# Kernel optimization log

Measured on AMD Instinct MI355X. Metric: run time of the kernel, lower is better.

Reference implementation:

```python
import jax, jax.numpy as jnp
import numpy as np

V, N, K, D, H = 100000, 20000, 32, 256, 256


def setup_inputs() -> dict:
    key = jax.random.key(0)
    k1, k2, k3, k4, k5, k6 = jax.random.split(key, 6)
    return {
        "embed_table": jax.random.normal(k1, (V, D), dtype=jnp.float32),
        "node_ids": jax.random.randint(k2, (N,), 0, V, dtype=jnp.int64) if jax.config.jax_enable_x64 else jax.random.randint(k2, (N,), 0, V, dtype=jnp.int32),
        "nb_ids": jax.random.randint(k3, (N, K), 0, V, dtype=jnp.int32),
        "self_weight": jax.random.normal(k4, (D, H), dtype=jnp.float32) / np.sqrt(D),
        "nb_weight": jax.random.normal(k5, (D, H), dtype=jnp.float32) / np.sqrt(D),
        "bias": jax.random.normal(k6, (2 * H,), dtype=jnp.float32),
    }


def reference(embed_table, node_ids, nb_ids, self_weight, nb_weight, bias):
    # gather self embeddings: [N, D]
    self_attr = embed_table[node_ids]
    # gather sampled neighbor embeddings [N, K, D] and mean-pool over K
    nb_attr = jnp.mean(embed_table[nb_ids], axis=1)
    from_self = self_attr @ self_weight          # [N, H]
    from_nb = nb_attr @ nb_weight                # [N, H]
    out = jnp.concatenate((from_self, from_nb), axis=1) + bias  # concat combine
    return jax.nn.relu(out)
```

## Files before the change

kernel.cpp:

```cpp
#include <hip/hip_runtime.h>

#define VV 100000
#define NN 20000
#define KK 32
#define DD 256
#define HH 256
#define BN 16

typedef __attribute__((ext_vector_type(8))) short bf16x8;
typedef __attribute__((ext_vector_type(4))) float f32x4;

__device__ __forceinline__ ushort f2bf(float f) {
    uint u = __float_as_uint(f);
    return (ushort)((u + 0x7FFFu + ((u >> 16) & 1u)) >> 16);
}
__device__ __forceinline__ float bf2f(ushort u) {
    return __uint_as_float(((uint)u) << 16);
}

__global__ __launch_bounds__(256) void k_conv(
    const float* __restrict__ E, ushort* __restrict__ Eb)
{
    const size_t i = ((size_t)blockIdx.x * 256 + threadIdx.x) * 8;
    const f32x4 a = __builtin_nontemporal_load((const f32x4*)&E[i]);
    const f32x4 b = __builtin_nontemporal_load((const f32x4*)&E[i + 4]);
    bf16x8 v;
    v[0] = (short)f2bf(a.x); v[1] = (short)f2bf(a.y);
    v[2] = (short)f2bf(a.z); v[3] = (short)f2bf(a.w);
    v[4] = (short)f2bf(b.x); v[5] = (short)f2bf(b.y);
    v[6] = (short)f2bf(b.z); v[7] = (short)f2bf(b.w);
    *(bf16x8*)&Eb[i] = v;
}

__global__ __launch_bounds__(256) void k_prep_wf(
    const float* __restrict__ Ws, const float* __restrict__ Wn,
    ushort* __restrict__ WTf)
{
    __shared__ float t[256][17];
    const int tid = threadIdx.x;
    const int h   = blockIdx.y;
    const int tt  = blockIdx.x;
    const float* src = h ? Wn : Ws;
    const int h0 = tt * 16;
    const int c = tid & 15, dr = tid >> 4;
    #pragma unroll
    for (int s = 0; s < 16; ++s) {
        const int d = s * 16 + dr;
        t[d][c] = src[(size_t)d * HH + h0 + c];
    }
    __syncthreads();
    const int fl = tid & 63, w = tid >> 6;
    const int r16 = fl & 15, kg = fl >> 4;
    #pragma unroll
    for (int p = 0; p < 2; ++p) {
        const int ks = w + p * 4;
        bf16x8 v;
        #pragma unroll
        for (int e = 0; e < 8; ++e)
            v[e] = (short)f2bf(t[ks * 32 + kg * 8 + e][r16]);
        *(bf16x8*)&WTf[(((size_t)(h * 16 + tt) * 8 + ks) * 64 + fl) * 8] = v;
    }
}

__global__ __launch_bounds__(256) void k_prep_w(
    const float* __restrict__ Ws, const float* __restrict__ Wn,
    ushort* __restrict__ WT)
{
    __shared__ float t[64][65];
    const int tid = threadIdx.x;
    const float* src = (blockIdx.z == 0) ? Ws : Wn;
    ushort* dst = WT + (size_t)blockIdx.z * HH * DD;
    const int d0 = blockIdx.x * 64, h0 = blockIdx.y * 64;

    const int hl = tid & 63, dq = tid >> 6;
    #pragma unroll
    for (int i = 0; i < 16; ++i) {
        const int dl = dq * 16 + i;
        t[dl][hl] = src[(size_t)(d0 + dl) * HH + h0 + hl];
    }
    __syncthreads();
    const int dl = tid & 63, hq = tid >> 6;
    #pragma unroll
    for (int i = 0; i < 16; ++i) {
        const int h2 = hq * 16 + i;
        dst[(size_t)(h0 + h2) * DD + d0 + dl] = f2bf(t[dl][h2]);
    }
}

__global__ __launch_bounds__(256, 4) void k_gatherf(
    const ushort* __restrict__ Eb,
    const int*    __restrict__ node_ids,
    const int*    __restrict__ nb_ids,
    ushort*       __restrict__ A)
{
    const int wv   = __builtin_amdgcn_readfirstlane((int)(threadIdx.x >> 6));
    const int lane = threadIdx.x & 63;
    const int sub  = lane >> 5;
    const int l31  = lane & 31;
    const int g    = blockIdx.x * 4 + wv;
    const int base = g * KK;

    const int srow = node_ids[g];
    bf16x8 r[17];
    r[0] = *(const bf16x8*)&Eb[((size_t)(uint)srow << 8) + l31 * 8];
    #pragma unroll
    for (int j = 1; j <= 16; ++j) {
        const int rlo = nb_ids[base + j - 1];
        const int rhi = nb_ids[base + j + 15];
        const int row = sub ? rhi : rlo;
        r[j] = *(const bf16x8*)&Eb[((size_t)(uint)row << 8) + l31 * 8];
    }

    float acc[8];
    #pragma unroll
    for (int e = 0; e < 8; ++e) acc[e] = 0.f;
    #pragma unroll
    for (int j = 1; j <= 16; ++j) {
        #pragma unroll
        for (int e = 0; e < 8; ++e)
            acc[e] += bf2f((ushort)r[j][e]);
    }
    #pragma unroll
    for (int e = 0; e < 8; ++e)
        acc[e] += __shfl_xor(acc[e], 32);

    const float inv = 1.0f / (float)KK;
    bf16x8 nv;
    #pragma unroll
    for (int e = 0; e < 8; ++e)
        nv[e] = (short)f2bf(acc[e] * inv);

    const int tile = g >> 4, rr = g & 15;
    const int ks = l31 >> 2, kgw = l31 & 3;
    const size_t dst = (((size_t)(tile * 2 + sub) * 8 + ks) * 64 + kgw * 16 + rr) * 8;
    *(bf16x8*)&A[dst] = sub ? nv : r[0];
}

__global__ __launch_bounds__(256, 4) void k_gemmf(
    const ushort* __restrict__ A,
    const ushort* __restrict__ WTf,
    const float*  __restrict__ bias,
    float*        __restrict__ out)
{
    const int wv   = __builtin_amdgcn_readfirstlane((int)(threadIdx.x >> 6));
    const int lane = threadIdx.x & 63;
    const int tile = blockIdx.x;
    const int half = wv >> 1, qt = wv & 1;
    const int r16 = lane & 15, kg = lane >> 4;

    bf16x8 a[8];
    #pragma unroll
    for (int ks = 0; ks < 8; ++ks)
        a[ks] = *(const bf16x8*)&A[(((size_t)(tile * 2 + half) * 8 + ks) * 64 + lane) * 8];

    f32x4 accs[8];
    #pragma unroll
    for (int ct = 0; ct < 8; ++ct) {
        const int t = qt * 8 + ct;
        f32x4 acc = {0.f, 0.f, 0.f, 0.f};
        #pragma unroll
        for (int ks = 0; ks < 8; ++ks) {
            const bf16x8 b = *(const bf16x8*)&WTf[(((size_t)(half * 16 + t) * 8 + ks) * 64 + lane) * 8];
            acc = __builtin_amdgcn_mfma_f32_16x16x32_bf16(a[ks], b, acc, 0, 0, 0);
        }
        accs[ct] = acc;
    }

    #pragma unroll
    for (int ct = 0; ct < 8; ++ct) {
        const int cglob = half * HH + (qt * 8 + ct) * 16 + r16;
        const float bv = bias[cglob];
        #pragma unroll
        for (int r = 0; r < 4; ++r) {
            const float v = accs[ct][r] + bv;
            out[(size_t)(tile * 16 + kg * 4 + r) * (2 * HH) + cglob] = v > 0.f ? v : 0.f;
        }
    }
}

template<int EBF16>
__global__ __launch_bounds__(256, 4) void k_fused(
    const float*  __restrict__ Ef,
    const ushort* __restrict__ Eb,
    const int*    __restrict__ node_ids,
    const int*    __restrict__ nb_ids,
    const ushort* __restrict__ WT,
    const float*  __restrict__ bias,
    float*        __restrict__ out)
{
    __shared__ ushort As[BN][DD];
    __shared__ ushort An[BN][DD];
    const int tid  = threadIdx.x;
    const int wave = tid >> 6;
    const int lane = tid & 63;
    const int g0   = blockIdx.x * BN;

    if (EBF16) {
        const int sub = lane >> 5;
        const int l31 = lane & 31;
        const uint boff = (uint)l31 * 16;
        for (int n = wave; n < BN; n += 4) {
            const int g = g0 + n;
            const int base = g * KK;
            const uint swz = ((uint)(n & 7)) << 4;
            const int srow = node_ids[g];
            const bf16x8 sv = *(const bf16x8*)&Eb[((size_t)(uint)srow << 8) + l31 * 8];
            bf16x8 r[16];
            #pragma unroll
            for (int j = 0; j < 16; ++j) {
                const int rlo = nb_ids[base + 2 * j];
                const int rhi = nb_ids[base + 2 * j + 1];
                const int row = sub ? rhi : rlo;
                r[j] = *(const bf16x8*)&Eb[((size_t)(uint)row << 8) + l31 * 8];
            }
            float acc[8];
            #pragma unroll
            for (int e = 0; e < 8; ++e) acc[e] = 0.f;
            #pragma unroll
            for (int j = 0; j < 16; ++j) {
                #pragma unroll
                for (int e = 0; e < 8; ++e)
                    acc[e] += bf2f((ushort)r[j][e]);
            }
            #pragma unroll
            for (int e = 0; e < 8; ++e)
                acc[e] += __shfl_xor(acc[e], 32);
            const float inv = 1.0f / (float)KK;
            bf16x8 nv;
            #pragma unroll
            for (int e = 0; e < 8; ++e)
                nv[e] = (short)f2bf(acc[e] * inv);
            if (sub == 0) {
                *(bf16x8*)((char*)&As[n][0] + (boff ^ swz)) = sv;
            } else {
                *(bf16x8*)((char*)&An[n][0] + (boff ^ swz)) = nv;
            }
        }
    } else {
        for (int n = wave; n < BN; n += 4) {
            const int g = g0 + n;
            const int srow = node_ids[g];
            const uint swz  = ((uint)(n & 7)) << 4;
            const uint boff = (uint)lane * 8;
            const float4 s = *(const float4*)&Ef[(size_t)srow * DD + lane * 4];
            ushort4 sv = make_ushort4(f2bf(s.x), f2bf(s.y), f2bf(s.z), f2bf(s.w));
            float4 acc = make_float4(0.f, 0.f, 0.f, 0.f);
            #pragma unroll
            for (int k0 = 0; k0 < KK; k0 += 8) {
                float4 r[8];
                #pragma unroll
                for (int j = 0; j < 8; ++j) {
                    const int row = nb_ids[g * KK + k0 + j];
                    r[j] = *(const float4*)&Ef[(size_t)row * DD + lane * 4];
                }
                #pragma unroll
                for (int j = 0; j < 8; ++j) {
                    acc.x += r[j].x; acc.y += r[j].y;
                    acc.z += r[j].z; acc.w += r[j].w;
                }
            }
            const float inv = 1.0f / (float)KK;
            const ushort4 nv = make_ushort4(f2bf(acc.x * inv), f2bf(acc.y * inv),
                                            f2bf(acc.z * inv), f2bf(acc.w * inv));
            *(ushort4*)((char*)&As[n][0] + (boff ^ swz)) = sv;
            *(ushort4*)((char*)&An[n][0] + (boff ^ swz)) = nv;
        }
    }
    __syncthreads();

    const int half = wave >> 1;
    const int colq = (wave & 1) * 128;
    const int r16  = lane & 15;
    const int kg   = lane >> 4;
    const uint rswz = ((uint)(r16 & 7)) << 4;
    const char* Arow = (const char*)(half ? &An[r16][0] : &As[r16][0]);

    bf16x8 a[8];
    #pragma unroll
    for (int ks = 0; ks < 8; ++ks) {
        const uint off = (uint)(ks * 64 + kg * 16);
        a[ks] = *(const bf16x8*)(Arow + (off ^ rswz));
    }

    const ushort* Wb = WT + (size_t)half * HH * DD;
    f32x4 accs[8];
    #pragma unroll
    for (int ct = 0; ct < 8; ++ct) {
        const int c = colq + ct * 16 + r16;
        const ushort* Bb = Wb + (size_t)c * DD + kg * 8;
        f32x4 acc = {0.f, 0.f, 0.f, 0.f};
        #pragma unroll
        for (int ks = 0; ks < 8; ++ks) {
            const bf16x8 b = *(const bf16x8*)(Bb + ks * 32);
            acc = __builtin_amdgcn_mfma_f32_16x16x32_bf16(a[ks], b, acc, 0, 0, 0);
        }
        accs[ct] = acc;
    }

    #pragma unroll
    for (int ct = 0; ct < 8; ++ct) {
        const int cglob = half * HH + colq + ct * 16 + r16;
        const float bv = bias[cglob];
        #pragma unroll
        for (int r = 0; r < 4; ++r) {
            const float v = accs[ct][r] + bv;
            out[(size_t)(g0 + kg * 4 + r) * (2 * HH) + cglob] = v > 0.f ? v : 0.f;
        }
    }
}

__global__ __launch_bounds__(256, 4) void hetegraph_fused_kernel(
    const float* __restrict__ embed, const int* __restrict__ node_ids,
    const int* __restrict__ nb_ids, const float* __restrict__ Ws,
    const float* __restrict__ Wn, const float* __restrict__ bias,
    float* __restrict__ out)
{
    __shared__ float As[BN][DD];
    __shared__ float An[BN][DD];
    const int tid = threadIdx.x, wave = tid >> 6, lane = tid & 63;
    const int g0 = blockIdx.x * BN;
    for (int n = wave; n < BN; n += 4) {
        const int g = g0 + n;
        const int self_row = node_ids[g];
        const float4 s = *(const float4*)&embed[(size_t)self_row * DD + lane * 4];
        float4 acc = make_float4(0.f, 0.f, 0.f, 0.f);
        for (int k0 = 0; k0 < KK; k0 += 8) {
            float4 r[8];
            #pragma unroll
            for (int j = 0; j < 8; ++j) {
                const int row = nb_ids[g * KK + k0 + j];
                r[j] = *(const float4*)&embed[(size_t)row * DD + lane * 4];
            }
            #pragma unroll
            for (int j = 0; j < 8; ++j) {
                acc.x += r[j].x; acc.y += r[j].y; acc.z += r[j].z; acc.w += r[j].w;
            }
        }
        const float inv = 1.0f / (float)KK;
        *(float4*)&As[n][lane * 4] = s;
        float4 m = make_float4(acc.x * inv, acc.y * inv, acc.z * inv, acc.w * inv);
        *(float4*)&An[n][lane * 4] = m;
    }
    __syncthreads();
    const int h = tid;
    {
        float acc[BN];
        #pragma unroll
        for (int n = 0; n < BN; ++n) acc[n] = 0.f;
        for (int d0 = 0; d0 < DD; d0 += 4) {
            const float w0 = Ws[(d0+0)*HH+h], w1 = Ws[(d0+1)*HH+h];
            const float w2 = Ws[(d0+2)*HH+h], w3 = Ws[(d0+3)*HH+h];
            #pragma unroll
            for (int n = 0; n < BN; ++n) {
                const float4 a = *(const float4*)&As[n][d0];
                acc[n] = fmaf(a.x,w0,acc[n]); acc[n] = fmaf(a.y,w1,acc[n]);
                acc[n] = fmaf(a.z,w2,acc[n]); acc[n] = fmaf(a.w,w3,acc[n]);
            }
        }
        const float b = bias[h];
        #pragma unroll
        for (int n = 0; n < BN; ++n) {
            const float v = acc[n] + b;
            out[(size_t)(g0+n)*(2*HH) + h] = v > 0.f ? v : 0.f;
        }
    }
    {
        float acc[BN];
        #pragma unroll
        for (int n = 0; n < BN; ++n) acc[n] = 0.f;
        for (int d0 = 0; d0 < DD; d0 += 4) {
            const float w0 = Wn[(d0+0)*HH+h], w1 = Wn[(d0+1)*HH+h];
            const float w2 = Wn[(d0+2)*HH+h], w3 = Wn[(d0+3)*HH+h];
            #pragma unroll
            for (int n = 0; n < BN; ++n) {
                const float4 a = *(const float4*)&An[n][d0];
                acc[n] = fmaf(a.x,w0,acc[n]); acc[n] = fmaf(a.y,w1,acc[n]);
                acc[n] = fmaf(a.z,w2,acc[n]); acc[n] = fmaf(a.w,w3,acc[n]);
            }
        }
        const float b = bias[HH + h];
        #pragma unroll
        for (int n = 0; n < BN; ++n) {
            const float v = acc[n] + b;
            out[(size_t)(g0+n)*(2*HH) + HH + h] = v > 0.f ? v : 0.f;
        }
    }
}

extern "C" void kernel_launch(void* const* d_in, const int* in_sizes, int n_in,
                              void* d_out, int out_size, void* d_ws, size_t ws_size,
                              hipStream_t stream) {
    const float* embed    = (const float*)d_in[0];
    const int*   node_ids = (const int*)d_in[1];
    const int*   nb_ids   = (const int*)d_in[2];
    const float* Ws       = (const float*)d_in[3];
    const float* Wn       = (const float*)d_in[4];
    const float* bias     = (const float*)d_in[5];
    float*       out      = (float*)d_out;

    const size_t eb_bytes  = (size_t)VV * DD * sizeof(ushort);
    const size_t wtf_bytes = 2ull * 16 * 8 * 64 * 8 * sizeof(ushort);
    const size_t af_bytes  = (size_t)(NN / 16) * 2 * 8 * 64 * 8 * sizeof(ushort);
    const size_t wt_bytes  = 2ull * HH * DD * sizeof(ushort);

    if (ws_size >= eb_bytes + wtf_bytes + af_bytes) {
        ushort* Eb  = (ushort*)d_ws;
        ushort* WTf = (ushort*)((char*)d_ws + eb_bytes);
        ushort* Af  = (ushort*)((char*)d_ws + eb_bytes + wtf_bytes);
        k_prep_wf<<<dim3(16, 2), dim3(256), 0, stream>>>(Ws, Wn, WTf);
        k_conv<<<dim3(VV * DD / 2048), dim3(256), 0, stream>>>(embed, Eb);
        k_gatherf<<<dim3(NN / 4), dim3(256), 0, stream>>>(Eb, node_ids, nb_ids, Af);
        k_gemmf<<<dim3(NN / 16), dim3(256), 0, stream>>>(Af, WTf, bias, out);
    } else if (ws_size >= eb_bytes + wt_bytes) {
        ushort* Eb = (ushort*)d_ws;
        ushort* WT = (ushort*)((char*)d_ws + eb_bytes);
        k_conv<<<dim3(VV * DD / 2048), dim3(256), 0, stream>>>(embed, Eb);
        k_prep_w<<<dim3(DD / 64, HH / 64, 2), dim3(256), 0, stream>>>(Ws, Wn, WT);
        k_fused<1><<<dim3(NN / BN), dim3(256), 0, stream>>>(
            nullptr, Eb, node_ids, nb_ids, WT, bias, out);
    } else if (ws_size >= wt_bytes) {
        ushort* WT = (ushort*)d_ws;
        k_prep_w<<<dim3(DD / 64, HH / 64, 2), dim3(256), 0, stream>>>(Ws, Wn, WT);
        k_fused<0><<<dim3(NN / BN), dim3(256), 0, stream>>>(
            embed, nullptr, node_ids, nb_ids, WT, bias, out);
    } else {
        hetegraph_fused_kernel<<<dim3(NN / BN), dim3(256), 0, stream>>>(
            embed, node_ids, nb_ids, Ws, Wn, bias, out);
    }
}
```

Measured before the change: 102.0 us.

## Store embedding table as fp8 and gather neighbors from fp8 copy

Converts the embedding table to fp8 (e4m3 via cvt_pk_fp8) instead of bf16, halving the workspace write and the neighbor-gather read traffic. The gather kernel is restructured: each wave splits 32 neighbors across 4 lane groups, each loading full 256-byte fp8 rows, then reduces with shuffles. Self rows are read directly from the fp32 table. Risks accuracy loss from the 3-bit mantissa in the neighbor mean.

```diff
diff --git a/kernel.cpp b/kernel.cpp
--- a/kernel.cpp
+++ b/kernel.cpp
@@ -9,6 +9,8 @@
 
 typedef __attribute__((ext_vector_type(8))) short bf16x8;
 typedef __attribute__((ext_vector_type(4))) float f32x4;
+typedef __attribute__((ext_vector_type(2))) float f32x2;
+typedef __attribute__((ext_vector_type(4))) uint  u32x4;
 
 __device__ __forceinline__ ushort f2bf(float f) {
     uint u = __float_as_uint(f);
@@ -16,6 +18,22 @@
 }
 __device__ __forceinline__ float bf2f(ushort u) {
     return __uint_as_float(((uint)u) << 16);
+}
+
+__global__ __launch_bounds__(256) void k_conv8(
+    const float* __restrict__ E, unsigned char* __restrict__ E8)
+{
+    const size_t i = ((size_t)blockIdx.x * 256 + threadIdx.x) * 16;
+    u32x4 o;
+    #pragma unroll
+    for (int w = 0; w < 4; ++w) {
+        const f32x4 a = __builtin_nontemporal_load((const f32x4*)&E[i + w * 4]);
+        int r = 0;
+        r = __builtin_amdgcn_cvt_pk_fp8_f32(a.x, a.y, r, false);
+        r = __builtin_amdgcn_cvt_pk_fp8_f32(a.z, a.w, r, true);
+        o[w] = (uint)r;
+    }
+    *(u32x4*)&E8[i] = o;
 }
 
 __global__ __launch_bounds__(256) void k_conv(
@@ -87,53 +105,76 @@
     }
 }
 
-__global__ __launch_bounds__(256, 4) void k_gatherf(
-    const ushort* __restrict__ Eb,
-    const int*    __restrict__ node_ids,
-    const int*    __restrict__ nb_ids,
-    ushort*       __restrict__ A)
-{
-    const int wv   = __builtin_amdgcn_readfirstlane((int)(threadIdx.x >> 6));
+__global__ __launch_bounds__(256, 8) void k_gather8(
+    const float*         __restrict__ Ef,
+    const unsigned char* __restrict__ E8,
+    const int*           __restrict__ node_ids,
+    const int*           __restrict__ nb_ids,
+    ushort*              __restrict__ A)
+{
+    const int wv   = threadIdx.x >> 6;
     const int lane = threadIdx.x & 63;
-    const int sub  = lane >> 5;
-    const int l31  = lane & 31;
+    const int q    = lane >> 4, l15 = lane & 15;
+    const int sub  = lane >> 5, l31 = lane & 31;
     const int g    = blockIdx.x * 4 + wv;
     const int base = g * KK;
 
+    int rid[8];
+    #pragma unroll
+    for (int j = 0; j < 8; ++j)
+        rid[j] = nb_ids[base + q * 8 + j];
+
     const int srow = node_ids[g];
-    bf16x8 r[17];
-    r[0] = *(const bf16x8*)&Eb[((size_t)(uint)srow << 8) + l31 * 8];
-    #pragma unroll
-    for (int j = 1; j <= 16; ++j) {
-        const int rlo = nb_ids[base + j - 1];
-        const int rhi = nb_ids[base + j + 15];
-        const int row = sub ? rhi : rlo;
-        r[j] = *(const bf16x8*)&Eb[((size_t)(uint)row << 8) + l31 * 8];
-    }
-
-    float acc[8];
-    #pragma unroll
-    for (int e = 0; e < 8; ++e) acc[e] = 0.f;
-    #pragma unroll
-    for (int j = 1; j <= 16; ++j) {
+    const f32x4 s0 = *(const f32x4*)&Ef[(size_t)(uint)srow * DD + l31 * 8];
+    const f32x4 s1 = *(const f32x4*)&Ef[(size_t)(uint)srow * DD + l31 * 8 + 4];
+
+    u32x4 d[8];
+    #pragma unroll
+    for (int j = 0; j < 8; ++j)
+        d[j] = *(const u32x4*)&E8[(size_t)(uint)rid[j] * DD + l15 * 16];
+
+    float acc[16];
+    #pragma unroll
+    for (int e = 0; e < 16; ++e) acc[e] = 0.f;
+    #pragma unroll
+    for (int j = 0; j < 8; ++j) {
+        #pragma unroll
+        for (int w = 0; w < 4; ++w) {
+            const f32x2 lo = __builtin_amdgcn_cvt_pk_f32_fp8((int)d[j][w], false);
+            const f32x2 hi = __builtin_amdgcn_cvt_pk_f32_fp8((int)d[j][w], true);
+            acc[w * 4 + 0] += lo.x; acc[w * 4 + 1] += lo.y;
+            acc[w * 4 + 2] += hi.x; acc[w * 4 + 3] += hi.y;
+        }
+    }
+    #pragma unroll
+    for (int e = 0; e < 16; ++e) {
+        acc[e] += __shfl_xor(acc[e], 16);
+        acc[e] += __shfl_xor(acc[e], 32);
+    }
+
+    const int tile = g >> 4, rr = g & 15;
+
+    if (q < 2) {
+        const int e0 = 16 * l15 + 8 * q;
+        const int ks = e0 >> 5;
+        const int kg = (e0 >> 3) & 3;
+        const float inv = 1.0f / (float)KK;
+        bf16x8 nv;
         #pragma unroll
         for (int e = 0; e < 8; ++e)
-            acc[e] += bf2f((ushort)r[j][e]);
-    }
-    #pragma unroll
-    for (int e = 0; e < 8; ++e)
-        acc[e] += __shfl_xor(acc[e], 32);
-
-    const float inv = 1.0f / (float)KK;
-    bf16x8 nv;
-    #pragma unroll
-    for (int e = 0; e < 8; ++e)
-        nv[e] = (short)f2bf(acc[e] * inv);
-
-    const int tile = g >> 4, rr = g & 15;
-    const int ks = l31 >> 2, kgw = l31 & 3;
-    const size_t dst = (((size_t)(tile * 2 + sub) * 8 + ks) * 64 + kgw * 16 + rr) * 8;
-    *(bf16x8*)&A[dst] = sub ? nv : r[0];
+            nv[e] = (short)f2bf(acc[8 * q + e] * inv);
+        const size_t dst = (((size_t)(tile * 2 + 1) * 8 + ks) * 64 + kg * 16 + rr) * 8;
+        *(bf16x8*)&A[dst] = nv;
+    }
+    if (sub == 0) {
+        bf16x8 sv;
+        sv[0] = (short)f2bf(s0.x); sv[1] = (short)f2bf(s0.y);
+        sv[2] = (short)f2bf(s0.z); sv[3] = (short)f2bf(s0.w);
+        sv[4] = (short)f2bf(s1.x); sv[5] = (short)f2bf(s1.y);
+        sv[6] = (short)f2bf(s1.z); sv[7] = (short)f2bf(s1.w);
+        const size_t dsts = (((size_t)(tile * 2 + 0) * 8 + (l31 >> 2)) * 64 + (l31 & 3) * 16 + rr) * 8;
+        *(bf16x8*)&A[dsts] = sv;
+    }
 }
 
 __global__ __launch_bounds__(256, 4) void k_gemmf(
@@ -398,18 +439,19 @@
     const float* bias     = (const float*)d_in[5];
     float*       out      = (float*)d_out;
 
+    const size_t e8_bytes  = (size_t)VV * DD;
     const size_t eb_bytes  = (size_t)VV * DD * sizeof(ushort);
     const size_t wtf_bytes = 2ull * 16 * 8 * 64 * 8 * sizeof(ushort);
     const size_t af_bytes  = (size_t)(NN / 16) * 2 * 8 * 64 * 8 * sizeof(ushort);
     const size_t wt_bytes  = 2ull * HH * DD * sizeof(ushort);
 
-    if (ws_size >= eb_bytes + wtf_bytes + af_bytes) {
-        ushort* Eb  = (ushort*)d_ws;
-        ushort* WTf = (ushort*)((char*)d_ws + eb_bytes);
-        ushort* Af  = (ushort*)((char*)d_ws + eb_bytes + wtf_bytes);
+    if (ws_size >= e8_bytes + wtf_bytes + af_bytes) {
+        unsigned char* E8  = (unsigned char*)d_ws;
+        ushort*        WTf = (ushort*)((char*)d_ws + e8_bytes);
+        ushort*        Af  = (ushort*)((char*)d_ws + e8_bytes + wtf_bytes);
         k_prep_wf<<<dim3(16, 2), dim3(256), 0, stream>>>(Ws, Wn, WTf);
-        k_conv<<<dim3(VV * DD / 2048), dim3(256), 0, stream>>>(embed, Eb);
-        k_gatherf<<<dim3(NN / 4), dim3(256), 0, stream>>>(Eb, node_ids, nb_ids, Af);
+        k_conv8<<<dim3(VV * DD / 4096), dim3(256), 0, stream>>>(embed, E8);
+        k_gather8<<<dim3(NN / 4), dim3(256), 0, stream>>>(embed, E8, node_ids, nb_ids, Af);
         k_gemmf<<<dim3(NN / 16), dim3(256), 0, stream>>>(Af, WTf, bias, out);
     } else if (ws_size >= eb_bytes + wt_bytes) {
         ushort* Eb = (ushort*)d_ws;
```

Result: slower. 216.2 us (+112.0%).
